# Kernel optimization log

Hardware: AMD Instinct MI355X
Metric: run time of the kernel (lower is better)

Reference implementation:

```python
import jax, jax.numpy as jnp
import numpy as np

B, S, D_MODEL, NUM_HEADS, MAX_LEN = 4, 1024, 1024, 16, 1024
D_HEAD = D_MODEL // NUM_HEADS


def _skew(QEr):
    # QEr: (b, h, s, s). Music-Transformer skew: pad one col on the left,
    # reshape swapping the last two dims, drop the first row.
    b, h, r, c = QEr.shape
    padded = jnp.pad(QEr, ((0, 0), (0, 0), (0, 0), (1, 0)))  # (b,h,r,c+1)
    reshaped = padded.reshape(b, h, c + 1, r)
    return reshaped[:, :, 1:, :]  # (b,h,s,s)


def setup_inputs() -> dict:
    key = jax.random.key(0)
    ks = jax.random.split(key, 8)
    sc = 1.0 / np.sqrt(D_MODEL).astype(np.float32)
    return {
        "x": jax.random.normal(ks[0], (B, S, D_MODEL), jnp.float32),
        "Wq": jax.random.normal(ks[1], (D_MODEL, D_MODEL), jnp.float32) * sc,
        "bq": jnp.zeros((D_MODEL,), jnp.float32),
        "Wk": jax.random.normal(ks[2], (D_MODEL, D_MODEL), jnp.float32) * sc,
        "bk": jnp.zeros((D_MODEL,), jnp.float32),
        "Wv": jax.random.normal(ks[3], (D_MODEL, D_MODEL), jnp.float32) * sc,
        "bv": jnp.zeros((D_MODEL,), jnp.float32),
        "Er": jax.random.normal(ks[4], (MAX_LEN, D_HEAD), jnp.float32),
    }


def reference(x, Wq, bq, Wk, bk, Wv, bv, Er):
    b, s, _ = x.shape
    h, dh = NUM_HEADS, D_HEAD
    # projections -> (b, h, s, dh). Weights stored [in, out] (equiv. to torch W.T).
    q = (x @ Wq + bq).reshape(b, s, h, dh).transpose(0, 2, 1, 3)
    k = (x @ Wk + bk).reshape(b, s, h, dh).transpose(0, 2, 1, 3)
    v = (x @ Wv + bv).reshape(b, s, h, dh).transpose(0, 2, 1, 3)
    Er_t = Er[MAX_LEN - s:, :]                      # (s, dh)
    QEr = jnp.einsum('bhsd,td->bhst', q, Er_t)      # (b,h,s,s)
    Srel = _skew(QEr)
    scores = (jnp.einsum('bhsd,bhtd->bhst', q, k) + Srel) / np.float32(np.sqrt(dh))
    causal = jnp.tril(jnp.ones((s, s), bool))       # (s,s)
    scores = jnp.where(causal[None, None], scores, -jnp.inf)
    attn = jax.nn.softmax(scores, axis=-1)
    out = jnp.einsum('bhst,bhtd->bhsd', attn, v)    # (b,h,s,dh)
    return out.transpose(0, 2, 1, 3).reshape(b, s, h * dh)
```

## Files before the change

### kernel.cpp

```cpp
#include <hip/hip_runtime.h>
#include <hip/hip_bf16.h>
#include <math.h>

typedef __attribute__((ext_vector_type(8))) short short8;
typedef __attribute__((ext_vector_type(4))) float f32x4;
typedef __attribute__((ext_vector_type(4))) unsigned short us4;
typedef __attribute__((ext_vector_type(2))) unsigned int u32x2;

#define DM 1024
#define NH 16
#define DH 64
#define SS 1024
#define C2 0.180336879f

#define GLDS16(g, l) __builtin_amdgcn_global_load_lds(                      \
    (const __attribute__((address_space(1))) unsigned int*)(g),             \
    (__attribute__((address_space(3))) unsigned int*)(l), 16, 0, 0)

__device__ __forceinline__ unsigned short f2b(float f){
    unsigned int u = __float_as_uint(f);
    u += 0x7fffu + ((u >> 16) & 1u);
    return (unsigned short)(u >> 16);
}
__device__ __forceinline__ float b2f(unsigned short b){
    return __uint_as_float(((unsigned int)b) << 16);
}
__device__ __forceinline__ unsigned int cvt_pk_bf16(float lo, float hi){
    unsigned int r;
    asm volatile("v_cvt_pk_bf16_f32 %0, %1, %2" : "=v"(r) : "v"(lo), "v"(hi));
    return r;
}

__global__ __launch_bounds__(256) void cast_f32_bf16_k(const float* __restrict__ in,
                                                       unsigned short* __restrict__ out){
    int i = (blockIdx.x * 256 + threadIdx.x) * 4;
    float4 v = *(const float4*)(in + i);
    us4 o = { f2b(v.x), f2b(v.y), f2b(v.z), f2b(v.w) };
    *(us4*)(out + i) = o;
}

__global__ __launch_bounds__(256) void transpose_cast_w_k(const float* __restrict__ Wq,
                                                          const float* __restrict__ Wk,
                                                          const float* __restrict__ Wv,
                                                          unsigned short* __restrict__ wT){
    __shared__ float tile[32][33];
    const float* W = blockIdx.z==0 ? Wq : (blockIdx.z==1 ? Wk : Wv);
    int o0 = blockIdx.x*32, k0 = blockIdx.y*32;
    int tx = threadIdx.x, ty = threadIdx.y;
    #pragma unroll
    for (int i=0;i<32;i+=8) tile[ty+i][tx] = W[(k0+ty+i)*DM + o0+tx];
    __syncthreads();
    #pragma unroll
    for (int i=0;i<32;i+=8) wT[(blockIdx.z*DM + o0+ty+i)*DM + k0+tx] = f2b(tile[tx][ty+i]);
}

__global__ __launch_bounds__(256) void gemm_qkv_k(
    const unsigned short* __restrict__ xb, const unsigned short* __restrict__ wT,
    const float* __restrict__ bq, const float* __restrict__ bk, const float* __restrict__ bv,
    unsigned short* __restrict__ Qb, unsigned short* __restrict__ Kb, unsigned short* __restrict__ Vb)
{
    __shared__ unsigned short lda[128*32];
    __shared__ unsigned short ldb[128*32];
    const int tid = threadIdx.x;
    const int lane = tid & 63, w = tid >> 6;
    const int wr = w >> 1, wc = w & 1;
    const int lr = lane & 15, lk = (lane >> 4) * 8, lk4 = lane >> 4;
    const int m0 = blockIdx.y * 128, n0 = blockIdx.x * 128;
    f32x4 acc[4][4] = {};
    for (int k0 = 0; k0 < DM; k0 += 32){
        #pragma unroll
        for (int p=0;p<2;p++){
            int idx = tid + p*256;
            int row = idx >> 2, cc = (idx & 3) * 8;
            GLDS16(&xb[(m0+row)*DM + k0 + cc], &lda[idx<<3]);
            GLDS16(&wT[(n0+row)*DM + k0 + cc], &ldb[idx<<3]);
        }
        __syncthreads();
        short8 a[4], b[4];
        #pragma unroll
        for (int m=0;m<4;m++) a[m] = *(const short8*)(&lda[(wr*64+m*16+lr)*32 + lk]);
        #pragma unroll
        for (int n=0;n<4;n++) b[n] = *(const short8*)(&ldb[(wc*64+n*16+lr)*32 + lk]);
        __builtin_amdgcn_s_setprio(1);
        #pragma unroll
        for (int m=0;m<4;m++)
            #pragma unroll
            for (int n=0;n<4;n++)
                acc[m][n] = __builtin_amdgcn_mfma_f32_16x16x32_bf16(a[m], b[n], acc[m][n], 0,0,0);
        __builtin_amdgcn_s_setprio(0);
        __syncthreads();
    }
    #pragma unroll
    for (int m=0;m<4;m++){
        #pragma unroll
        for (int n=0;n<4;n++){
            int C = n0 + wc*64 + n*16 + lr;
            int proj = C >> 10, hd = C & 1023;
            const float* bias = proj==0 ? bq : (proj==1 ? bk : bv);
            float badd = bias[hd];
            int h = hd >> 6, d = hd & 63;
            #pragma unroll
            for (int r=0;r<4;r++){
                int R = m0 + wr*64 + m*16 + lk4*4 + r;
                int b_ = R >> 10, s = R & 1023;
                float v = acc[m][n][r] + badd;
                unsigned short val = f2b(proj==0 ? v*C2 : v);
                unsigned short* dst = proj==0 ? Qb : (proj==1 ? Kb : Vb);
                dst[(((b_*NH)+h)*SS + s)*DH + d] = val;
            }
        }
    }
}

__global__ __launch_bounds__(256) void transpose_v_k(const unsigned short* __restrict__ Vb,
                                                     unsigned short* __restrict__ VTb){
    __shared__ unsigned short t[64*72];
    const int tid = threadIdx.x;
    const int bh = blockIdx.x, s0 = blockIdx.y * 64;
    const int s = tid & 63, d0 = (tid >> 6) * 16;
    const unsigned short* src = Vb + (bh*SS + s0 + s)*DH;
    short8 v0 = *(const short8*)(src + d0);
    short8 v1 = *(const short8*)(src + d0 + 8);
    #pragma unroll
    for (int e=0;e<8;e++){
        t[(d0+e)*72 + s]   = (unsigned short)v0[e];
        t[(d0+8+e)*72 + s] = (unsigned short)v1[e];
    }
    __syncthreads();
    unsigned short* dst = VTb + bh*DH*SS + s0;
    #pragma unroll
    for (int q=0;q<2;q++){
        int idx = q*256 + tid;
        int d = idx >> 3, sc = idx & 7;
        short8 o = *(const short8*)(&t[d*72 + sc*8]);
        *(short8*)(dst + d*SS + sc*8) = o;
    }
}

__global__ __launch_bounds__(512, 4) void attn_k(
    const unsigned short* __restrict__ Qb, const unsigned short* __restrict__ Kb,
    const unsigned short* __restrict__ VTb, const unsigned short* __restrict__ Erb,
    float* __restrict__ out)
{
    __shared__ unsigned short k_lds[64*64];
    __shared__ unsigned short vt_lds[64*64];
    __shared__ unsigned short er_lds[192*64];
    __shared__ unsigned short p_lds[128*64];
    __shared__ unsigned short rbt[80*136];

    const int tid = threadIdx.x, lane = tid & 63, w = tid >> 6;
    const int lr = lane & 15, lk4 = lane >> 4;
    const int bh = blockIdx.x;
    const int i0 = (int)(gridDim.y - 1 - blockIdx.y) * 128;
    const unsigned short* q_b  = Qb  + bh*SS*DH;
    const unsigned short* k_b  = Kb  + bh*SS*DH;
    const unsigned short* vt_b = VTb + bh*DH*SS;

    auto STAGE_K = [&](int j0){
        int row = tid >> 3, ch = tid & 7;
        GLDS16(&k_b[(j0+row)*DH + ((ch ^ (row&7))<<3)], &k_lds[tid<<3]);
    };
    auto STAGE_VT = [&](int j0){
        int row = tid >> 3, ch = tid & 7;
        GLDS16(&vt_b[row*SS + j0 + ((ch ^ (row&7))<<3)], &vt_lds[tid<<3]);
    };
    auto STAGE_ER = [&](int t0){
        #pragma unroll
        for (int p=0;p<3;p++){
            int idx = tid + p*512;
            int row = idx >> 3, ch = idx & 7;
            GLDS16(&Erb[(t0+row)*DH + ((ch ^ (row&7))<<3)], &er_lds[idx<<3]);
        }
    };

    const int ntiles = i0/64 + 2;
    STAGE_K(0);
    STAGE_ER(896 - i0);

    short8 qf[2];
    #pragma unroll
    for (int kk=0;kk<2;kk++)
        qf[kk] = *(const short8*)(&q_b[(i0 + w*16 + lr)*DH + kk*32 + lk4*8]);

    __syncthreads();

    f32x4 o_acc[4] = {};
    float l_r[4] = {0.f,0.f,0.f,0.f};
    const int fbase = 7 - w;

    for (int t=0; t<ntiles; t++){
        const int j0 = t*64;
        STAGE_VT(j0);

        f32x4 s_acc[4] = {};
        f32x4 r_acc[5] = {};
        __builtin_amdgcn_s_setprio(1);
        #pragma unroll
        for (int kk=0;kk<2;kk++){
            const int sco = ((kk*4+lk4) ^ (lr&7)) << 3;
            #pragma unroll
            for (int n=0;n<4;n++){
                short8 kf = *(const short8*)(&k_lds[(n*16+lr)*64 + sco]);
                s_acc[n] = __builtin_amdgcn_mfma_f32_16x16x32_bf16(qf[kk], kf, s_acc[n], 0,0,0);
            }
            #pragma unroll
            for (int fi=0;fi<5;fi++){
                short8 ef = *(const short8*)(&er_lds[((fbase+fi)*16+lr)*64 + sco]);
                r_acc[fi] = __builtin_amdgcn_mfma_f32_16x16x32_bf16(qf[kk], ef, r_acc[fi], 0,0,0);
            }
        }
        __builtin_amdgcn_s_setprio(0);

        __syncthreads();
        if (t+1 < ntiles){
            STAGE_K(j0+64);
            STAGE_ER(896 - i0 + j0 + 64);
        }

        #pragma unroll
        for (int fi=0;fi<5;fi++){
            u32x2 pk;
            pk[0] = cvt_pk_bf16(r_acc[fi][0], r_acc[fi][1]);
            pk[1] = cvt_pk_bf16(r_acc[fi][2], r_acc[fi][3]);
            *(u32x2*)(&rbt[(fi*16+lr)*136 + w*16 + lk4*4]) = pk;
        }

        float s2[4][4];
        #pragma unroll
        for (int r=0;r<4;r++){
            const int rr = lk4*4 + r;
            const int gb = (15 - rr + lr)*136 + w*16 + rr;
            #pragma unroll
            for (int n=0;n<4;n++)
                s2[n][r] = s_acc[n][r] + b2f(rbt[gb + n*2176]);
        }
        if (t >= ntiles-2){
            #pragma unroll
            for (int r=0;r<4;r++){
                const int gi = i0 + w*16 + lk4*4 + r;
                #pragma unroll
                for (int n=0;n<4;n++)
                    if (j0 + n*16 + lr > gi) s2[n][r] = -INFINITY;
            }
        }
        #pragma unroll
        for (int r=0;r<4;r++){
            float p0 = __builtin_amdgcn_exp2f(s2[0][r]);
            float p1 = __builtin_amdgcn_exp2f(s2[1][r]);
            float p2 = __builtin_amdgcn_exp2f(s2[2][r]);
            float p3 = __builtin_amdgcn_exp2f(s2[3][r]);
            l_r[r] += (p0+p1)+(p2+p3);
            unsigned int u01 = cvt_pk_bf16(p0, p1);
            unsigned int u23 = cvt_pk_bf16(p2, p3);
            const int li = w*16 + lk4*4 + r;
            const int ro = li*64 + (lr&7);
            p_lds[ro + (((0 + (lr>>3)) ^ (li&7))<<3)] = (unsigned short)u01;
            p_lds[ro + (((2 + (lr>>3)) ^ (li&7))<<3)] = (unsigned short)(u01>>16);
            p_lds[ro + (((4 + (lr>>3)) ^ (li&7))<<3)] = (unsigned short)u23;
            p_lds[ro + (((6 + (lr>>3)) ^ (li&7))<<3)] = (unsigned short)(u23>>16);
        }

        __builtin_amdgcn_s_setprio(1);
        #pragma unroll
        for (int kk=0;kk<2;kk++){
            const int sco = ((kk*4+lk4) ^ (lr&7)) << 3;
            short8 pf = *(const short8*)(&p_lds[(w*16+lr)*64 + sco]);
            #pragma unroll
            for (int n=0;n<4;n++){
                short8 vf = *(const short8*)(&vt_lds[(n*16+lr)*64 + sco]);
                o_acc[n] = __builtin_amdgcn_mfma_f32_16x16x32_bf16(pf, vf, o_acc[n], 0,0,0);
            }
        }
        __builtin_amdgcn_s_setprio(0);
        __syncthreads();
    }

    #pragma unroll
    for (int r=0;r<4;r++){
        float l = l_r[r];
        #pragma unroll
        for (int msk=1; msk<16; msk<<=1) l += __shfl_xor(l, msk);
        l_r[r] = 1.0f / l;
    }
    const int b_ = bh >> 4, h = bh & 15;
    #pragma unroll
    for (int n=0;n<4;n++)
        #pragma unroll
        for (int r=0;r<4;r++){
            int li = w*16 + lk4*4 + r;
            int d = n*16 + lr;
            out[(b_*SS + i0 + li)*DM + h*DH + d] = o_acc[n][r] * l_r[r];
        }
}

extern "C" void kernel_launch(void* const* d_in, const int* in_sizes, int n_in,
                              void* d_out, int out_size, void* d_ws, size_t ws_size,
                              hipStream_t stream)
{
    const float* x  = (const float*)d_in[0];
    const float* Wq = (const float*)d_in[1];
    const float* bq = (const float*)d_in[2];
    const float* Wk = (const float*)d_in[3];
    const float* bk = (const float*)d_in[4];
    const float* Wv = (const float*)d_in[5];
    const float* bv = (const float*)d_in[6];
    const float* Er = (const float*)d_in[7];
    float* out = (float*)d_out;
    char* ws = (char*)d_ws;
    unsigned short* xb  = (unsigned short*)(ws);
    unsigned short* wT  = (unsigned short*)(ws + 8388608);
    unsigned short* erb = (unsigned short*)(ws + 14680064);
    unsigned short* Qb  = (unsigned short*)(ws + 14827520);
    unsigned short* Kb  = (unsigned short*)(ws + 23216128);
    unsigned short* Vb  = (unsigned short*)(ws + 31604736);
    unsigned short* VTb = xb;

    cast_f32_bf16_k<<<4096, 256, 0, stream>>>(x, xb);
    cast_f32_bf16_k<<<64, 256, 0, stream>>>(Er, erb);
    hipMemsetAsync(erb + 1024*DH, 0, 128*DH*sizeof(unsigned short), stream);
    transpose_cast_w_k<<<dim3(32,32,3), dim3(32,8), 0, stream>>>(Wq, Wk, Wv, wT);
    gemm_qkv_k<<<dim3(24,32), 256, 0, stream>>>(xb, wT, bq, bk, bv, Qb, Kb, Vb);
    transpose_v_k<<<dim3(64,16), 256, 0, stream>>>(Vb, VTb);
    attn_k<<<dim3(64,8), 512, 0, stream>>>(Qb, Kb, VTb, erb, out);
}
```

Measured before the change: 97.54 us.

## Load Er fragments directly to registers and drop Er LDS staging

Removes the shared-memory staging buffer for the relative-position table Er and has each wave load its five Er fragments straight from global memory into registers every tile. This frees 24 KB of LDS and removes the LDS write and read traffic for Er, which allows launch bounds to raise the occupancy hint from 4 to 6 blocks. The rbt row stride also changes from 136 to 134, likely to reduce bank conflicts. In exchange each tile issues uncoalesced-ish global loads with exposed latency and more register pressure, and neighbouring waves redundantly read overlapping Er rows.

```diff
diff --git a/kernel.cpp b/kernel.cpp
--- a/kernel.cpp
+++ b/kernel.cpp
@@ -12,6 +12,7 @@
 #define DH 64
 #define SS 1024
 #define C2 0.180336879f
+#define RBS 134
 
 #define GLDS16(g, l) __builtin_amdgcn_global_load_lds(                      \
     (const __attribute__((address_space(1))) unsigned int*)(g),             \
@@ -137,16 +138,15 @@
     }
 }
 
-__global__ __launch_bounds__(512, 4) void attn_k(
+__global__ __launch_bounds__(512, 6) void attn_k(
     const unsigned short* __restrict__ Qb, const unsigned short* __restrict__ Kb,
     const unsigned short* __restrict__ VTb, const unsigned short* __restrict__ Erb,
     float* __restrict__ out)
 {
     __shared__ unsigned short k_lds[64*64];
     __shared__ unsigned short vt_lds[64*64];
-    __shared__ unsigned short er_lds[192*64];
     __shared__ unsigned short p_lds[128*64];
-    __shared__ unsigned short rbt[80*136];
+    __shared__ unsigned short rbt[80*RBS];
 
     const int tid = threadIdx.x, lane = tid & 63, w = tid >> 6;
     const int lr = lane & 15, lk4 = lane >> 4;
@@ -164,33 +164,34 @@
         int row = tid >> 3, ch = tid & 7;
         GLDS16(&vt_b[row*SS + j0 + ((ch ^ (row&7))<<3)], &vt_lds[tid<<3]);
     };
-    auto STAGE_ER = [&](int t0){
-        #pragma unroll
-        for (int p=0;p<3;p++){
-            int idx = tid + p*512;
-            int row = idx >> 3, ch = idx & 7;
-            GLDS16(&Erb[(t0+row)*DH + ((ch ^ (row&7))<<3)], &er_lds[idx<<3]);
-        }
-    };
 
     const int ntiles = i0/64 + 2;
     STAGE_K(0);
-    STAGE_ER(896 - i0);
 
     short8 qf[2];
     #pragma unroll
     for (int kk=0;kk<2;kk++)
         qf[kk] = *(const short8*)(&q_b[(i0 + w*16 + lr)*DH + kk*32 + lk4*8]);
 
+    const int fbase = 7 - w;
+    const unsigned short* er_w = Erb + (896 - i0 + fbase*16 + lr)*DH + lk4*8;
+
     __syncthreads();
 
     f32x4 o_acc[4] = {};
     float l_r[4] = {0.f,0.f,0.f,0.f};
-    const int fbase = 7 - w;
 
     for (int t=0; t<ntiles; t++){
         const int j0 = t*64;
         STAGE_VT(j0);
+
+        const unsigned short* ep = er_w + j0*DH;
+        short8 efr[2][5];
+        #pragma unroll
+        for (int fi=0;fi<5;fi++)
+            #pragma unroll
+            for (int kk=0;kk<2;kk++)
+                efr[kk][fi] = *(const short8*)(ep + fi*16*DH + kk*32);
 
         f32x4 s_acc[4] = {};
         f32x4 r_acc[5] = {};
@@ -204,35 +205,31 @@
                 s_acc[n] = __builtin_amdgcn_mfma_f32_16x16x32_bf16(qf[kk], kf, s_acc[n], 0,0,0);
             }
             #pragma unroll
-            for (int fi=0;fi<5;fi++){
-                short8 ef = *(const short8*)(&er_lds[((fbase+fi)*16+lr)*64 + sco]);
-                r_acc[fi] = __builtin_amdgcn_mfma_f32_16x16x32_bf16(qf[kk], ef, r_acc[fi], 0,0,0);
-            }
+            for (int fi=0;fi<5;fi++)
+                r_acc[fi] = __builtin_amdgcn_mfma_f32_16x16x32_bf16(qf[kk], efr[kk][fi], r_acc[fi], 0,0,0);
         }
         __builtin_amdgcn_s_setprio(0);
 
         __syncthreads();
-        if (t+1 < ntiles){
+        if (t+1 < ntiles)
             STAGE_K(j0+64);
-            STAGE_ER(896 - i0 + j0 + 64);
-        }
 
         #pragma unroll
         for (int fi=0;fi<5;fi++){
             u32x2 pk;
             pk[0] = cvt_pk_bf16(r_acc[fi][0], r_acc[fi][1]);
             pk[1] = cvt_pk_bf16(r_acc[fi][2], r_acc[fi][3]);
-            *(u32x2*)(&rbt[(fi*16+lr)*136 + w*16 + lk4*4]) = pk;
+            *(u32x2*)(&rbt[(fi*16+lr)*RBS + w*16 + lk4*4]) = pk;
         }
 
         float s2[4][4];
         #pragma unroll
         for (int r=0;r<4;r++){
             const int rr = lk4*4 + r;
-            const int gb = (15 - rr + lr)*136 + w*16 + rr;
+            const int gb = (15 - rr + lr)*RBS + w*16 + rr;
             #pragma unroll
             for (int n=0;n<4;n++)
-                s2[n][r] = s_acc[n][r] + b2f(rbt[gb + n*2176]);
+                s2[n][r] = s_acc[n][r] + b2f(rbt[gb + n*16*RBS]);
         }
         if (t >= ntiles-2){
             #pragma unroll
```

New measurement: 233.2 us. +139.1%, slower.
